# Kernel optimization log

Hardware: AMD Instinct MI355X
Metric: run time of the kernel (lower is better)

## Reference

```python
import jax, jax.numpy as jnp
import numpy as np

N, DIM = 8192, 128
NEG = -1e9  # finite stand-in for -inf; exp underflows to 0 for masked entries


def setup_inputs() -> dict:
    key = jax.random.key(0)
    k1, k2, k3, k4 = jax.random.split(key, 4)
    h = jax.random.normal(k1, (N, DIM), dtype=jnp.float32)
    social_adj = jax.random.randint(k2, (N, N), 0, 2, dtype=jnp.int32)
    # nn.Linear(dim, dim, bias=False): weight [out, in]; xavier-ish scale
    W = jax.random.normal(k3, (DIM, DIM), dtype=jnp.float32) / np.sqrt(DIM)
    a = jax.random.normal(k4, (2 * DIM,), dtype=jnp.float32) / np.sqrt(2 * DIM)
    return {"h": h, "social_adj": social_adj, "W": W, "a": a}


def reference(h, social_adj, W, a):
    Wh = h @ W.T                              # [N, d]
    d = Wh.shape[1]
    a1 = Wh @ a[:d]                           # [N]
    a2 = Wh @ a[d:]                           # [N]
    e = jax.nn.leaky_relu(a1[:, None] + a2[None, :], negative_slope=0.2)  # [N, N]
    mask = social_adj != 0
    e = jnp.where(mask, e, NEG)
    alpha = jax.nn.softmax(e, axis=-1)        # [N, N]
    # rows with no neighbors: torch gives nan->0 via nan_to_num; we zero them directly
    no_neighbor = ~jnp.any(mask, axis=-1)     # [N]
    alpha = jnp.where(no_neighbor[:, None], 0.0, alpha)
    out = alpha @ Wh                          # [N, d]; already 0 on no_neighbor rows
    return out, alpha
```

## Files before the change

### kernel.cpp

```cpp
#include <hip/hip_runtime.h>
#include <hip/hip_bf16.h>

#define NN 8192
#define DIM 128
#define RPB 8
#define KC 256

typedef __attribute__((ext_vector_type(8))) short bf16x8;
typedef __attribute__((ext_vector_type(4))) float f32x4;
typedef __attribute__((ext_vector_type(4))) int i32x4;
typedef __attribute__((ext_vector_type(4))) unsigned int u32x4;
typedef __attribute__((ext_vector_type(4))) unsigned short u16x4;
typedef __attribute__((ext_vector_type(4))) short s16x4;

static __device__ inline unsigned short f2bf(float x) {
    __hip_bfloat16 b = __float2bfloat16(x);
    return *reinterpret_cast<unsigned short*>(&b);
}

struct BSplit { short hi, lo; };
static __device__ inline BSplit bsplit(float x) {
    BSplit r;
    __hip_bfloat16 h = __float2bfloat16(x);
    r.hi = *reinterpret_cast<short*>(&h);
    float rem = x - __bfloat162float(h);
    __hip_bfloat16 l = __float2bfloat16(rem);
    r.lo = *reinterpret_cast<short*>(&l);
    return r;
}

__global__ __launch_bounds__(256) void k1m(const float* __restrict__ h,
                                           const float* __restrict__ W,
                                           const float* __restrict__ a,
                                           __hip_bfloat16* __restrict__ whbT,
                                           float* __restrict__ a1g,
                                           unsigned* __restrict__ pku) {
    __shared__ short whi[128 * 132];
    __shared__ short wlo[128 * 132];
    __shared__ short wt[8 * 128 * 8];
    __shared__ float a_sh[256];

    const int tid = threadIdx.x;
    const int wv = tid >> 6, lane = tid & 63;
    const int r0 = blockIdx.x * 64;

    for (int idx = tid; idx < 128 * 128; idx += 256) {
        const int d = idx >> 7, k = idx & 127;
        BSplit s = bsplit(W[idx]);
        whi[d * 132 + k] = s.hi;
        wlo[d * 132 + k] = s.lo;
    }
    a_sh[tid] = a[tid];
    __syncthreads();

    f32x4 acc[8];
    #pragma unroll
    for (int n = 0; n < 8; ++n) acc[n] = (f32x4){0.f, 0.f, 0.f, 0.f};

    const int arow = r0 + wv * 16 + (lane & 15);
    const int ksub = (lane >> 4) * 8;
    const float* hp = h + (size_t)arow * DIM + ksub;

    #pragma unroll
    for (int kk = 0; kk < 128; kk += 32) {
        f32x4 x0 = *(const f32x4*)(hp + kk);
        f32x4 x1 = *(const f32x4*)(hp + kk + 4);
        bf16x8 ah, al;
        {
            BSplit s0 = bsplit(x0.x), s1 = bsplit(x0.y), s2 = bsplit(x0.z), s3 = bsplit(x0.w);
            BSplit s4 = bsplit(x1.x), s5 = bsplit(x1.y), s6 = bsplit(x1.z), s7 = bsplit(x1.w);
            ah[0] = s0.hi; al[0] = s0.lo; ah[1] = s1.hi; al[1] = s1.lo;
            ah[2] = s2.hi; al[2] = s2.lo; ah[3] = s3.hi; al[3] = s3.lo;
            ah[4] = s4.hi; al[4] = s4.lo; ah[5] = s5.hi; al[5] = s5.lo;
            ah[6] = s6.hi; al[6] = s6.lo; ah[7] = s7.hi; al[7] = s7.lo;
        }
        #pragma unroll
        for (int n = 0; n < 8; ++n) {
            const int boff = (n * 16 + (lane & 15)) * 132 + kk + ksub;
            bf16x8 bh = *(const bf16x8*)(whi + boff);
            bf16x8 bl = *(const bf16x8*)(wlo + boff);
            acc[n] = __builtin_amdgcn_mfma_f32_16x16x32_bf16(ah, bh, acc[n], 0, 0, 0);
            acc[n] = __builtin_amdgcn_mfma_f32_16x16x32_bf16(ah, bl, acc[n], 0, 0, 0);
            acc[n] = __builtin_amdgcn_mfma_f32_16x16x32_bf16(al, bh, acc[n], 0, 0, 0);
        }
    }

    float p1[4] = {0.f, 0.f, 0.f, 0.f}, p2[4] = {0.f, 0.f, 0.f, 0.f};
    #pragma unroll
    for (int n = 0; n < 8; ++n) {
        const float av1 = a_sh[n * 16 + (lane & 15)];
        const float av2 = a_sh[128 + n * 16 + (lane & 15)];
        #pragma unroll
        for (int q = 0; q < 4; ++q) {
            p1[q] += acc[n][q] * av1;
            p2[q] += acc[n][q] * av2;
        }
    }
    #pragma unroll
    for (int o = 8; o >= 1; o >>= 1) {
        #pragma unroll
        for (int q = 0; q < 4; ++q) {
            p1[q] += __shfl_xor(p1[q], o, 64);
            p2[q] += __shfl_xor(p2[q], o, 64);
        }
    }
    if ((lane & 15) == 0) {
        #pragma unroll
        for (int q = 0; q < 4; ++q) {
            const int row = r0 + wv * 16 + (lane >> 4) * 4 + q;
            a1g[row] = p1[q];
            const float E1v = expf(p2[q]);
            const float E2v = expf(0.2f * p2[q]);
            pku[row] = (unsigned)f2bf(E1v) | ((unsigned)f2bf(E2v) << 16);
        }
    }

    #pragma unroll
    for (int n = 0; n < 8; ++n) {
        #pragma unroll
        for (int q = 0; q < 4; ++q) {
            const int kloc = wv * 16 + (lane >> 4) * 4 + q;
            const int d = n * 16 + (lane & 15);
            wt[(kloc >> 3) * 1024 + d * 8 + (kloc & 7)] = (short)f2bf(acc[n][q]);
        }
    }
    __syncthreads();
    short* dst = reinterpret_cast<short*>(whbT) + ((size_t)r0 << 7);
    for (int idx = tid * 4; idx < 8192; idx += 1024)
        *(s16x4*)(dst + idx) = *(const s16x4*)(wt + idx);
}

static __device__ inline void sa_group(const i32x4 v, const u32x4 tb,
                                       const float T, const int lane,
                                       float& s1, float& s2,
                                       unsigned* bgrp) {
    unsigned long long m0 = __ballot(v.x != 0);
    unsigned long long m1 = __ballot(v.y != 0);
    unsigned long long m2 = __ballot(v.z != 0);
    unsigned long long m3 = __ballot(v.w != 0);
    if (lane == 0) {
        u32x4 w;
        w.x = (unsigned)m0; w.y = (unsigned)m1;
        w.z = (unsigned)m2; w.w = (unsigned)m3;
        *(u32x4*)(bgrp) = w;
    } else if (lane == 32) {
        u32x4 w;
        w.x = (unsigned)(m0 >> 32); w.y = (unsigned)(m1 >> 32);
        w.z = (unsigned)(m2 >> 32); w.w = (unsigned)(m3 >> 32);
        *(u32x4*)(bgrp + 4) = w;
    }
    float e1, e2; bool px;
    e1 = __uint_as_float(tb.x << 16); e2 = __uint_as_float(tb.x & 0xffff0000u);
    px = (e1 >= T);
    s1 += (v.x && px) ? e1 : 0.f;  s2 += (v.x && !px) ? e2 : 0.f;
    e1 = __uint_as_float(tb.y << 16); e2 = __uint_as_float(tb.y & 0xffff0000u);
    px = (e1 >= T);
    s1 += (v.y && px) ? e1 : 0.f;  s2 += (v.y && !px) ? e2 : 0.f;
    e1 = __uint_as_float(tb.z << 16); e2 = __uint_as_float(tb.z & 0xffff0000u);
    px = (e1 >= T);
    s1 += (v.z && px) ? e1 : 0.f;  s2 += (v.z && !px) ? e2 : 0.f;
    e1 = __uint_as_float(tb.w << 16); e2 = __uint_as_float(tb.w & 0xffff0000u);
    px = (e1 >= T);
    s1 += (v.w && px) ? e1 : 0.f;  s2 += (v.w && !px) ? e2 : 0.f;
}

__global__ __launch_bounds__(512, 8) void fs(const int* __restrict__ adj,
                                             const float* __restrict__ a1g,
                                             const unsigned* __restrict__ pku,
                                             const __hip_bfloat16* __restrict__ whbT,
                                             float* __restrict__ alpha,
                                             float* __restrict__ out) {
    __shared__ unsigned bmL[RPB][256];
    __shared__ __hip_bfloat16 abuf[2][16][KC + 8];
    __shared__ float crowL[RPB][4];

    const int tid = threadIdx.x;
    const int wv = tid >> 6, lane = tid & 63;
    const int r0 = blockIdx.x * RPB;

    #pragma unroll
    for (int b = 0; b < 2; ++b) {
        unsigned* pz = (unsigned*)&abuf[b][8][0];
        for (int idx = tid; idx < 4 * (KC + 8); idx += 512) pz[idx] = 0;
    }

    {
        const int gi = r0 + wv;
        const float a1i = a1g[gi];
        const float T = expf(-a1i);
        const int* arow = adj + (size_t)gi * NN;
        float s1 = 0.f, s2 = 0.f;
        for (int it = 0; it < NN / 512; ++it) {
            const int j0 = it * 512 + lane * 4;
            i32x4 v0 = __builtin_nontemporal_load((const i32x4*)(arow + j0));
            i32x4 v1 = __builtin_nontemporal_load((const i32x4*)(arow + j0 + 256));
            u32x4 t0 = *(const u32x4*)(pku + j0);
            u32x4 t1 = *(const u32x4*)(pku + j0 + 256);
            sa_group(v0, t0, T, lane, s1, s2, &bmL[wv][it * 16]);
            sa_group(v1, t1, T, lane, s1, s2, &bmL[wv][it * 16 + 8]);
        }
        #pragma unroll
        for (int o = 32; o >= 1; o >>= 1) {
            s1 += __shfl_xor(s1, o, 64);
            s2 += __shfl_xor(s2, o, 64);
        }
        if (lane == 0) {
            float c1 = 0.f, c2 = 0.f;
            if (s1 + s2 > 0.f) {
                float e1v = expf(a1i);
                float e2v = expf(0.2f * a1i);
                float S = e1v * s1 + e2v * s2;
                c1 = e1v / S;
                c2 = e2v / S;
            }
            crowL[wv][0] = c1; crowL[wv][1] = c2; crowL[wv][2] = T;
        }
    }
    __syncthreads();

    const float c1 = crowL[wv][0], c2 = crowL[wv][1], Tb = crowL[wv][2];
    f32x4 acc = (f32x4){0.f, 0.f, 0.f, 0.f};
    const int n0 = wv * 16;
    const short* wb = reinterpret_cast<const short*>(whbT);
    const short* bbase = wb + (size_t)(n0 + (lane & 15)) * 8 + (size_t)(lane >> 4) * 1024;
    float* arow_out = alpha + (size_t)(r0 + wv) * NN;
    const unsigned pbit = lane & 31;

    for (int kc = 0; kc < NN; kc += KC) {
        const int dbuf = (kc >> 8) & 1;
        const int j = kc + lane * 4;
        const int wbw = ((j >> 8) << 3) + (((j >> 7) & 1) << 2);
        u32x4 tb = *(const u32x4*)(pku + j);
        u32x4 w4 = *(const u32x4*)(&bmL[wv][wbw]);
        float e1c[4], e2c[4];
        e1c[0] = __uint_as_float(tb.x << 16); e2c[0] = __uint_as_float(tb.x & 0xffff0000u);
        e1c[1] = __uint_as_float(tb.y << 16); e2c[1] = __uint_as_float(tb.y & 0xffff0000u);
        e1c[2] = __uint_as_float(tb.z << 16); e2c[2] = __uint_as_float(tb.z & 0xffff0000u);
        e1c[3] = __uint_as_float(tb.w << 16); e2c[3] = __uint_as_float(tb.w & 0xffff0000u);
        f32x4 al;
        al.x = ((w4.x >> pbit) & 1) ? ((e1c[0] >= Tb) ? c1 * e1c[0] : c2 * e2c[0]) : 0.f;
        al.y = ((w4.y >> pbit) & 1) ? ((e1c[1] >= Tb) ? c1 * e1c[1] : c2 * e2c[1]) : 0.f;
        al.z = ((w4.z >> pbit) & 1) ? ((e1c[2] >= Tb) ? c1 * e1c[2] : c2 * e2c[2]) : 0.f;
        al.w = ((w4.w >> pbit) & 1) ? ((e1c[3] >= Tb) ? c1 * e1c[3] : c2 * e2c[3]) : 0.f;
        __builtin_nontemporal_store(al, (f32x4*)(arow_out + j));
        u16x4 ub4;
        ub4.x = f2bf(al.x); ub4.y = f2bf(al.y); ub4.z = f2bf(al.z); ub4.w = f2bf(al.w);
        *(u16x4*)(&abuf[dbuf][wv][lane * 4]) = ub4;
        __syncthreads();
        #pragma unroll
        for (int kk = 0; kk < KC; kk += 32) {
            bf16x8 bf = *(const bf16x8*)(bbase + (size_t)((kc + kk) >> 3) * 1024);
            bf16x8 af = *(const bf16x8*)(&abuf[dbuf][lane & 15][kk + 8 * (lane >> 4)]);
            acc = __builtin_amdgcn_mfma_f32_16x16x32_bf16(af, bf, acc, 0, 0, 0);
        }
    }

    const int rl = (lane >> 4) * 4;
    if (rl < RPB) {
        #pragma unroll
        for (int q = 0; q < 4; ++q)
            out[(size_t)(r0 + rl + q) * DIM + n0 + (lane & 15)] = acc[q];
    }
}

extern "C" void kernel_launch(void* const* d_in, const int* in_sizes, int n_in,
                              void* d_out, int out_size, void* d_ws, size_t ws_size,
                              hipStream_t stream) {
    const float* h   = (const float*)d_in[0];
    const int*   adj = (const int*)d_in[1];
    const float* W   = (const float*)d_in[2];
    const float* a   = (const float*)d_in[3];

    float* out   = (float*)d_out;
    float* alpha = out + (size_t)NN * DIM;

    char* ws = (char*)d_ws;
    __hip_bfloat16* whbT = (__hip_bfloat16*)(ws);
    float* a1g    = (float*)(ws + 0x200000);
    unsigned* pku = (unsigned*)(ws + 0x208000);

    k1m<<<NN / 64, 256, 0, stream>>>(h, W, a, whbT, a1g, pku);
    fs<<<NN / RPB, 512, 0, stream>>>(adj, a1g, pku, whbT, alpha, out);
}
```

Before: 161.5 us.

## Halve block to 4 waves, each handling two rows and two output column tiles

```diff
diff --git a/kernel.cpp b/kernel.cpp
--- a/kernel.cpp
+++ b/kernel.cpp
@@ -164,7 +164,7 @@
     s1 += (v.w && px) ? e1 : 0.f;  s2 += (v.w && !px) ? e2 : 0.f;
 }
 
-__global__ __launch_bounds__(512, 8) void fs(const int* __restrict__ adj,
+__global__ __launch_bounds__(256, 6) void fs(const int* __restrict__ adj,
                                              const float* __restrict__ a1g,
                                              const unsigned* __restrict__ pku,
                                              const __hip_bfloat16* __restrict__ whbT,
@@ -181,11 +181,13 @@
     #pragma unroll
     for (int b = 0; b < 2; ++b) {
         unsigned* pz = (unsigned*)&abuf[b][8][0];
-        for (int idx = tid; idx < 4 * (KC + 8); idx += 512) pz[idx] = 0;
-    }
-
-    {
-        const int gi = r0 + wv;
+        for (int idx = tid; idx < 4 * (KC + 8); idx += 256) pz[idx] = 0;
+    }
+
+    #pragma unroll
+    for (int rr = 0; rr < 2; ++rr) {
+        const int r = wv * 2 + rr;
+        const int gi = r0 + r;
         const float a1i = a1g[gi];
         const float T = expf(-a1i);
         const int* arow = adj + (size_t)gi * NN;
@@ -196,8 +198,8 @@
             i32x4 v1 = __builtin_nontemporal_load((const i32x4*)(arow + j0 + 256));
             u32x4 t0 = *(const u32x4*)(pku + j0);
             u32x4 t1 = *(const u32x4*)(pku + j0 + 256);
-            sa_group(v0, t0, T, lane, s1, s2, &bmL[wv][it * 16]);
-            sa_group(v1, t1, T, lane, s1, s2, &bmL[wv][it * 16 + 8]);
+            sa_group(v0, t0, T, lane, s1, s2, &bmL[r][it * 16]);
+            sa_group(v1, t1, T, lane, s1, s2, &bmL[r][it * 16 + 8]);
         }
         #pragma unroll
         for (int o = 32; o >= 1; o >>= 1) {
@@ -213,17 +215,22 @@
                 c1 = e1v / S;
                 c2 = e2v / S;
             }
-            crowL[wv][0] = c1; crowL[wv][1] = c2; crowL[wv][2] = T;
+            crowL[r][0] = c1; crowL[r][1] = c2; crowL[r][2] = T;
         }
     }
     __syncthreads();
 
-    const float c1 = crowL[wv][0], c2 = crowL[wv][1], Tb = crowL[wv][2];
-    f32x4 acc = (f32x4){0.f, 0.f, 0.f, 0.f};
-    const int n0 = wv * 16;
+    float c1r[2], c2r[2], Tr[2];
+    #pragma unroll
+    for (int rr = 0; rr < 2; ++rr) {
+        const int r = wv * 2 + rr;
+        c1r[rr] = crowL[r][0]; c2r[rr] = crowL[r][1]; Tr[rr] = crowL[r][2];
+    }
+    f32x4 acc0 = (f32x4){0.f, 0.f, 0.f, 0.f};
+    f32x4 acc1 = (f32x4){0.f, 0.f, 0.f, 0.f};
+    const int n0 = wv * 32;
     const short* wb = reinterpret_cast<const short*>(whbT);
     const short* bbase = wb + (size_t)(n0 + (lane & 15)) * 8 + (size_t)(lane >> 4) * 1024;
-    float* arow_out = alpha + (size_t)(r0 + wv) * NN;
     const unsigned pbit = lane & 31;
 
     for (int kc = 0; kc < NN; kc += KC) {
@@ -231,35 +238,45 @@
         const int j = kc + lane * 4;
         const int wbw = ((j >> 8) << 3) + (((j >> 7) & 1) << 2);
         u32x4 tb = *(const u32x4*)(pku + j);
-        u32x4 w4 = *(const u32x4*)(&bmL[wv][wbw]);
         float e1c[4], e2c[4];
         e1c[0] = __uint_as_float(tb.x << 16); e2c[0] = __uint_as_float(tb.x & 0xffff0000u);
         e1c[1] = __uint_as_float(tb.y << 16); e2c[1] = __uint_as_float(tb.y & 0xffff0000u);
         e1c[2] = __uint_as_float(tb.z << 16); e2c[2] = __uint_as_float(tb.z & 0xffff0000u);
         e1c[3] = __uint_as_float(tb.w << 16); e2c[3] = __uint_as_float(tb.w & 0xffff0000u);
-        f32x4 al;
-        al.x = ((w4.x >> pbit) & 1) ? ((e1c[0] >= Tb) ? c1 * e1c[0] : c2 * e2c[0]) : 0.f;
-        al.y = ((w4.y >> pbit) & 1) ? ((e1c[1] >= Tb) ? c1 * e1c[1] : c2 * e2c[1]) : 0.f;
-        al.z = ((w4.z >> pbit) & 1) ? ((e1c[2] >= Tb) ? c1 * e1c[2] : c2 * e2c[2]) : 0.f;
-        al.w = ((w4.w >> pbit) & 1) ? ((e1c[3] >= Tb) ? c1 * e1c[3] : c2 * e2c[3]) : 0.f;
-        __builtin_nontemporal_store(al, (f32x4*)(arow_out + j));
-        u16x4 ub4;
-        ub4.x = f2bf(al.x); ub4.y = f2bf(al.y); ub4.z = f2bf(al.z); ub4.w = f2bf(al.w);
-        *(u16x4*)(&abuf[dbuf][wv][lane * 4]) = ub4;
+        #pragma unroll
+        for (int rr = 0; rr < 2; ++rr) {
+            const int r = wv * 2 + rr;
+            u32x4 w4 = *(const u32x4*)(&bmL[r][wbw]);
+            const float c1 = c1r[rr], c2 = c2r[rr], T = Tr[rr];
+            f32x4 al;
+            al.x = ((w4.x >> pbit) & 1) ? ((e1c[0] >= T) ? c1 * e1c[0] : c2 * e2c[0]) : 0.f;
+            al.y = ((w4.y >> pbit) & 1) ? ((e1c[1] >= T) ? c1 * e1c[1] : c2 * e2c[1]) : 0.f;
+            al.z = ((w4.z >> pbit) & 1) ? ((e1c[2] >= T) ? c1 * e1c[2] : c2 * e2c[2]) : 0.f;
+            al.w = ((w4.w >> pbit) & 1) ? ((e1c[3] >= T) ? c1 * e1c[3] : c2 * e2c[3]) : 0.f;
+            __builtin_nontemporal_store(al, (f32x4*)(alpha + (size_t)(r0 + r) * NN + j));
+            u16x4 ub4;
+            ub4.x = f2bf(al.x); ub4.y = f2bf(al.y); ub4.z = f2bf(al.z); ub4.w = f2bf(al.w);
+            *(u16x4*)(&abuf[dbuf][r][lane * 4]) = ub4;
+        }
         __syncthreads();
         #pragma unroll
         for (int kk = 0; kk < KC; kk += 32) {
-            bf16x8 bf = *(const bf16x8*)(bbase + (size_t)((kc + kk) >> 3) * 1024);
+            const short* bp = bbase + (size_t)((kc + kk) >> 3) * 1024;
+            bf16x8 b0 = *(const bf16x8*)(bp);
+            bf16x8 b1 = *(const bf16x8*)(bp + 128);
             bf16x8 af = *(const bf16x8*)(&abuf[dbuf][lane & 15][kk + 8 * (lane >> 4)]);
-            acc = __builtin_amdgcn_mfma_f32_16x16x32_bf16(af, bf, acc, 0, 0, 0);
+            acc0 = __builtin_amdgcn_mfma_f32_16x16x32_bf16(af, b0, acc0, 0, 0, 0);
+            acc1 = __builtin_amdgcn_mfma_f32_16x16x32_bf16(af, b1, acc1, 0, 0, 0);
         }
     }
 
     const int rl = (lane >> 4) * 4;
     if (rl < RPB) {
         #pragma unroll
-        for (int q = 0; q < 4; ++q)
-            out[(size_t)(r0 + rl + q) * DIM + n0 + (lane & 15)] = acc[q];
+        for (int q = 0; q < 4; ++q) {
+            out[(size_t)(r0 + rl + q) * DIM + n0 + (lane & 15)] = acc0[q];
+            out[(size_t)(r0 + rl + q) * DIM + n0 + 16 + (lane & 15)] = acc1[q];
+        }
     }
 }
 
@@ -280,5 +297,5 @@
     unsigned* pku = (unsigned*)(ws + 0x208000);
 
     k1m<<<NN / 64, 256, 0, stream>>>(h, W, a, whbT, a1g, pku);
-    fs<<<NN / RPB, 512, 0, stream>>>(adj, a1g, pku, whbT, alpha, out);
-}
+    fs<<<NN / RPB, 256, 0, stream>>>(adj, a1g, pku, whbT, alpha, out);
+}
```

New measurement: 153.7 us. -4.8%, faster.
